# Kernel tuning notes

Measured on AMD Instinct MI355X. Metric: run time of the kernel, lower is better.

## Reference

```python
import jax, jax.numpy as jnp
import numpy as np

N, D, H, C, ED, E = 50000, 128, 8, 16, 16, 800000  # nodes, model dim, heads, head dim, edge dim, edges

def _layer_norm(x, g, b, eps=1e-5):
    mu = x.mean(-1, keepdims=True)
    var = ((x - mu) ** 2).mean(-1, keepdims=True)
    return (x - mu) * jax.lax.rsqrt(var + eps) * g + b

def setup_inputs() -> dict:
    key = jax.random.key(0)
    ks = jax.random.split(key, 24)
    s = 0.05
    inp = {
        'x': jax.random.normal(ks[0], (N, D), jnp.float32),
        'edge_index': jax.random.randint(ks[1], (2, E), 0, N, jnp.int32),
        'edge_attr': jax.random.normal(ks[2], (E, ED), jnp.float32),
        # TransformerConv params (Linear convention: y = x @ W + b)
        'wq': s * jax.random.normal(ks[3], (D, H * C)), 'bq': s * jax.random.normal(ks[4], (H * C,)),
        'wk': s * jax.random.normal(ks[5], (D, H * C)), 'bk': s * jax.random.normal(ks[6], (H * C,)),
        'wv': s * jax.random.normal(ks[7], (D, H * C)), 'bv': s * jax.random.normal(ks[8], (H * C,)),
        'we': s * jax.random.normal(ks[9], (ED, H * C)),            # lin_edge, bias=False
        'wskip': s * jax.random.normal(ks[10], (D, H * C)), 'bskip': s * jax.random.normal(ks[11], (H * C,)),
        'wbeta': s * jax.random.normal(ks[12], (3 * H * C, 1)),     # lin_beta, bias=False
        # norms
        'ln1_g': 1.0 + s * jax.random.normal(ks[13], (D,)), 'ln1_b': s * jax.random.normal(ks[14], (D,)),
        'ln2_g': 1.0 + s * jax.random.normal(ks[15], (D,)), 'ln2_b': s * jax.random.normal(ks[16], (D,)),
        # FFN
        'w1': s * jax.random.normal(ks[17], (D, 2 * D)), 'b1': s * jax.random.normal(ks[18], (2 * D,)),
        'w2': s * jax.random.normal(ks[19], (2 * D, D)), 'b2': s * jax.random.normal(ks[20], (D,)),
    }
    return inp

def reference(x, edge_index, edge_attr, wq, bq, wk, bk, wv, bv, we, wskip, bskip, wbeta,
              ln1_g, ln1_b, ln2_g, ln2_b, w1, b1, w2, b2):
    src, dst = edge_index[0], edge_index[1]  # message flows src (j) -> dst (i)
    # --- pre-norm + TransformerConv (beta=True, concat=True, eval-mode dropout=identity) ---
    xn = _layer_norm(x, ln1_g, ln1_b)
    q = (xn @ wq + bq).reshape(N, H, C)
    k = (xn @ wk + bk).reshape(N, H, C)
    v = (xn @ wv + bv).reshape(N, H, C)
    e = (edge_attr @ we).reshape(E, H, C)
    kj = k[src] + e                                     # [E,H,C]
    alpha = (q[dst] * kj).sum(-1) / jnp.sqrt(jnp.float32(C))  # [E,H]
    # segment softmax over incoming edges per destination node
    m = jax.ops.segment_max(alpha, dst, num_segments=N)        # [N,H]
    ea = jnp.exp(alpha - m[dst])
    denom = jax.ops.segment_sum(ea, dst, num_segments=N)
    alpha = ea / (denom[dst] + 1e-16)
    msg = (v[src] + e) * alpha[..., None]               # [E,H,C]
    out = jax.ops.segment_sum(msg, dst, num_segments=N).reshape(N, H * C)
    # beta-gated skip
    x_r = xn @ wskip + bskip
    beta = jax.nn.sigmoid(jnp.concatenate([out, x_r, out - x_r], axis=-1) @ wbeta)  # [N,1]
    out = beta * x_r + (1.0 - beta) * out
    x = x + out
    # --- pre-norm FFN ---
    h = _layer_norm(x, ln2_g, ln2_b)
    h = jax.nn.gelu(h @ w1 + b1, approximate=False) @ w2 + b2
    return x + h
```

## Files before the change

### kernel.cpp

```cpp
#include <hip/hip_runtime.h>
#include <math.h>

#define N_NODES 50000
#define D_MODEL 128
#define N_HEADS 8
#define HEAD_C 16
#define E_DIM 16
#define N_EDGES 800000

typedef __attribute__((ext_vector_type(8))) short bf16x8;
typedef __attribute__((ext_vector_type(4))) float f32x4;

__device__ inline ushort f2bf(float f) {
    unsigned u = __float_as_uint(f);
    unsigned r = (u + 0x7fffu + ((u >> 16) & 1u)) >> 16;
    return (ushort)r;
}
__device__ inline float bf2f(ushort h) { return __uint_as_float(((unsigned)h) << 16); }
__device__ inline uint pack2(float a, float b) {
    return (uint)f2bf(a) | ((uint)f2bf(b) << 16);
}
__device__ inline float gelu_f(float v) {
    return 0.5f * v * (1.0f + erff(v * 0.70710678118654752f));
}

__global__ void prep_weights(const float* __restrict__ wq, const float* __restrict__ wk,
                             const float* __restrict__ wv, const float* __restrict__ wsk,
                             const float* __restrict__ bq, const float* __restrict__ bk,
                             const float* __restrict__ bv, const float* __restrict__ bsk,
                             const float* __restrict__ w1, const float* __restrict__ w2,
                             ushort* __restrict__ wqkvsT, float* __restrict__ bqkvs,
                             ushort* __restrict__ w1T, ushort* __restrict__ w2T)
{
    int idx = blockIdx.x * 256 + threadIdx.x;
    {
        int m = idx >> 7, kk = idx & 127;
        int b = m >> 7, ch = m & 127;
        const float* src = (b == 0) ? wq : (b == 1) ? wk : (b == 2) ? wv : wsk;
        wqkvsT[idx] = f2bf(src[kk * 128 + ch]);
    }
    if (idx < 256 * 128) {
        int m = idx >> 7, k = idx & 127;
        w1T[idx] = f2bf(w1[k * 256 + m]);
    }
    if (idx < 128 * 256) {
        int m = idx >> 8, k = idx & 255;
        w2T[idx] = f2bf(w2[k * 128 + m]);
    }
    if (idx < 512) {
        int b = idx >> 7, ch = idx & 127;
        const float* bb = (b == 0) ? bq : (b == 1) ? bk : (b == 2) ? bv : bsk;
        bqkvs[idx] = bb[ch];
    }
}

__global__ __launch_bounds__(256) void proj_ln_gemm(
    const float* __restrict__ X, const float* __restrict__ ln_g, const float* __restrict__ ln_b,
    const ushort* __restrict__ WT, const float* __restrict__ bias,
    ushort* __restrict__ Y, int nrows)
{
    __shared__ __align__(16) ushort Al[128 * 128];
    __shared__ __align__(16) ushort Wl[64 * 128];
    int tid = threadIdx.x;
    int wv = tid >> 6, lane = tid & 63;
    int row0 = blockIdx.x * 128;
    int col0 = blockIdx.y * 64;

    int c16 = tid & 15;
    float4 g0 = *(const float4*)&ln_g[c16 * 8];
    float4 g1 = *(const float4*)&ln_g[c16 * 8 + 4];
    float4 bb0 = *(const float4*)&ln_b[c16 * 8];
    float4 bb1 = *(const float4*)&ln_b[c16 * 8 + 4];

    #pragma unroll
    for (int i = 0; i < 8; ++i) {
        int c = tid + i * 256;
        int r = c >> 4;
        int gr = row0 + r;
        float4 xa = make_float4(0.f, 0.f, 0.f, 0.f), xb = xa;
        if (gr < nrows) {
            xa = *(const float4*)&X[(size_t)gr * 128 + c16 * 8];
            xb = *(const float4*)&X[(size_t)gr * 128 + c16 * 8 + 4];
        }
        float s  = xa.x + xa.y + xa.z + xa.w + xb.x + xb.y + xb.z + xb.w;
        float ss = xa.x*xa.x + xa.y*xa.y + xa.z*xa.z + xa.w*xa.w
                 + xb.x*xb.x + xb.y*xb.y + xb.z*xb.z + xb.w*xb.w;
        #pragma unroll
        for (int m = 1; m < 16; m <<= 1) {
            s  += __shfl_xor(s,  m, 64);
            ss += __shfl_xor(ss, m, 64);
        }
        float mu  = s * (1.0f / 128.0f);
        float var = ss * (1.0f / 128.0f) - mu * mu;
        float rs  = rsqrtf(var + 1e-5f);
        ushort h[8];
        h[0] = f2bf((xa.x - mu) * rs * g0.x + bb0.x);
        h[1] = f2bf((xa.y - mu) * rs * g0.y + bb0.y);
        h[2] = f2bf((xa.z - mu) * rs * g0.z + bb0.z);
        h[3] = f2bf((xa.w - mu) * rs * g0.w + bb0.w);
        h[4] = f2bf((xb.x - mu) * rs * g1.x + bb1.x);
        h[5] = f2bf((xb.y - mu) * rs * g1.y + bb1.y);
        h[6] = f2bf((xb.z - mu) * rs * g1.z + bb1.z);
        h[7] = f2bf((xb.w - mu) * rs * g1.w + bb1.w);
        int byte = r * 256 + ((c16 * 16) ^ ((r & 7) << 4));
        *(ulonglong2*)((char*)Al + byte) = *(ulonglong2*)h;
    }
    #pragma unroll
    for (int i = 0; i < 4; ++i) {
        int c = tid + i * 256;
        int r = c >> 4, cc = c & 15;
        ulonglong2 val = *(const ulonglong2*)(WT + (size_t)(col0 + r) * 128 + cc * 8);
        int byte = r * 256 + ((cc * 16) ^ ((r & 7) << 4));
        *(ulonglong2*)((char*)Wl + byte) = val;
    }
    __syncthreads();

    f32x4 acc[2][4];
    #pragma unroll
    for (int i = 0; i < 2; ++i)
        #pragma unroll
        for (int j = 0; j < 4; ++j) acc[i][j] = (f32x4){0.f, 0.f, 0.f, 0.f};
    #pragma unroll
    for (int ks = 0; ks < 4; ++ks) {
        bf16x8 af[2], bfr[4];
        #pragma unroll
        for (int rt = 0; rt < 2; ++rt) {
            int r = wv * 32 + rt * 16 + (lane & 15);
            int byte = r * 256 + ((ks * 64 + (lane >> 4) * 16) ^ ((r & 7) << 4));
            af[rt] = *(const bf16x8*)((const char*)Al + byte);
        }
        #pragma unroll
        for (int ct = 0; ct < 4; ++ct) {
            int r = ct * 16 + (lane & 15);
            int byte = r * 256 + ((ks * 64 + (lane >> 4) * 16) ^ ((r & 7) << 4));
            bfr[ct] = *(const bf16x8*)((const char*)Wl + byte);
        }
        #pragma unroll
        for (int rt = 0; rt < 2; ++rt)
            #pragma unroll
            for (int ct = 0; ct < 4; ++ct)
                acc[rt][ct] = __builtin_amdgcn_mfma_f32_16x16x32_bf16(
                    af[rt], bfr[ct], acc[rt][ct], 0, 0, 0);
    }
    #pragma unroll
    for (int rt = 0; rt < 2; ++rt) {
        #pragma unroll
        for (int ct = 0; ct < 4; ++ct) {
            int gcol = col0 + ct * 16 + (lane & 15);
            float bv = bias[gcol];
            #pragma unroll
            for (int r = 0; r < 4; ++r) {
                int grow = row0 + wv * 32 + rt * 16 + (lane >> 4) * 4 + r;
                if (grow >= nrows) continue;
                Y[(size_t)grow * 512 + gcol] = f2bf(acc[rt][ct][r] + bv);
            }
        }
    }
}

__global__ __launch_bounds__(256) void ffn_fused(
    const ushort* __restrict__ A, const ushort* __restrict__ W1T,
    const ushort* __restrict__ W2T, const float* __restrict__ b1,
    const float* __restrict__ b2, const float* __restrict__ xnew,
    float* __restrict__ out, int nrows)
{
    __shared__ __align__(16) ushort Xl[128 * 128];
    __shared__ __align__(16) ushort Wl[64 * 256];
    __shared__ __align__(16) ushort Hl[128 * 256];
    int tid = threadIdx.x;
    int wv = tid >> 6, lane = tid & 63;
    int row0 = blockIdx.x * 128;

    #pragma unroll
    for (int i = 0; i < 8; ++i) {
        int c = tid + i * 256;
        int r = c >> 4, c16 = c & 15;
        int gr = row0 + r;
        ulonglong2 val = {0ull, 0ull};
        if (gr < nrows) val = *(const ulonglong2*)(A + (size_t)gr * 128 + c16 * 8);
        int byte = r * 256 + ((c16 * 16) ^ ((r & 7) << 4));
        *(ulonglong2*)((char*)Xl + byte) = val;
    }

    for (int h = 0; h < 2; ++h) {
        #pragma unroll
        for (int i = 0; i < 8; ++i) {
            int c = tid + i * 256;
            int r = c >> 4, c16 = c & 15;
            ulonglong2 val = *(const ulonglong2*)(W1T + (size_t)(h * 128 + r) * 128 + c16 * 8);
            int byte = r * 256 + ((c16 * 16) ^ ((r & 7) << 4));
            *(ulonglong2*)((char*)Wl + byte) = val;
        }
        __syncthreads();
        f32x4 acc1[2][8];
        #pragma unroll
        for (int i = 0; i < 2; ++i)
            #pragma unroll
            for (int j = 0; j < 8; ++j) acc1[i][j] = (f32x4){0.f, 0.f, 0.f, 0.f};
        #pragma unroll
        for (int ks = 0; ks < 4; ++ks) {
            bf16x8 af[2], bfr[8];
            #pragma unroll
            for (int rt = 0; rt < 2; ++rt) {
                int r = wv * 32 + rt * 16 + (lane & 15);
                int byte = r * 256 + ((ks * 64 + (lane >> 4) * 16) ^ ((r & 7) << 4));
                af[rt] = *(const bf16x8*)((const char*)Xl + byte);
            }
            #pragma unroll
            for (int ct = 0; ct < 8; ++ct) {
                int r = ct * 16 + (lane & 15);
                int byte = r * 256 + ((ks * 64 + (lane >> 4) * 16) ^ ((r & 7) << 4));
                bfr[ct] = *(const bf16x8*)((const char*)Wl + byte);
            }
            #pragma unroll
            for (int rt = 0; rt < 2; ++rt)
                #pragma unroll
                for (int ct = 0; ct < 8; ++ct)
                    acc1[rt][ct] = __builtin_amdgcn_mfma_f32_16x16x32_bf16(
                        af[rt], bfr[ct], acc1[rt][ct], 0, 0, 0);
        }
        #pragma unroll
        for (int rt = 0; rt < 2; ++rt) {
            #pragma unroll
            for (int ct = 0; ct < 8; ++ct) {
                int col = h * 128 + ct * 16 + (lane & 15);
                float bv = b1[col];
                #pragma unroll
                for (int r = 0; r < 4; ++r) {
                    int row = wv * 32 + rt * 16 + (lane >> 4) * 4 + r;
                    float v = gelu_f(acc1[rt][ct][r] + bv);
                    int cb = col * 2;
                    int byte = row * 512 + (((cb) & ~15) ^ ((row & 7) << 4)) + (cb & 15);
                    *(ushort*)((char*)Hl + byte) = f2bf(v);
                }
            }
        }
        __syncthreads();
    }

    for (int g = 0; g < 2; ++g) {
        #pragma unroll
        for (int i = 0; i < 8; ++i) {
            int c = tid + i * 256;
            int r = c >> 5, c32 = c & 31;
            ulonglong2 val = *(const ulonglong2*)(W2T + (size_t)(g * 64 + r) * 256 + c32 * 8);
            int byte = r * 512 + ((c32 * 16) ^ ((r & 7) << 4));
            *(ulonglong2*)((char*)Wl + byte) = val;
        }
        __syncthreads();
        f32x4 acc2[2][4];
        #pragma unroll
        for (int i = 0; i < 2; ++i)
            #pragma unroll
            for (int j = 0; j < 4; ++j) acc2[i][j] = (f32x4){0.f, 0.f, 0.f, 0.f};
        #pragma unroll
        for (int ks = 0; ks < 8; ++ks) {
            bf16x8 af[2], bfr[4];
            #pragma unroll
            for (int rt = 0; rt < 2; ++rt) {
                int row = wv * 32 + rt * 16 + (lane & 15);
                int byte = row * 512 + ((ks * 64 + (lane >> 4) * 16) ^ ((row & 7) << 4));
                af[rt] = *(const bf16x8*)((const char*)Hl + byte);
            }
            #pragma unroll
            for (int ct = 0; ct < 4; ++ct) {
                int r = ct * 16 + (lane & 15);
                int byte = r * 512 + ((ks * 64 + (lane >> 4) * 16) ^ ((r & 7) << 4));
                bfr[ct] = *(const bf16x8*)((const char*)Wl + byte);
            }
            #pragma unroll
            for (int rt = 0; rt < 2; ++rt)
                #pragma unroll
                for (int ct = 0; ct < 4; ++ct)
                    acc2[rt][ct] = __builtin_amdgcn_mfma_f32_16x16x32_bf16(
                        af[rt], bfr[ct], acc2[rt][ct], 0, 0, 0);
        }
        #pragma unroll
        for (int rt = 0; rt < 2; ++rt) {
            #pragma unroll
            for (int ct = 0; ct < 4; ++ct) {
                int gcol = g * 64 + ct * 16 + (lane & 15);
                float bv = b2[gcol];
                #pragma unroll
                for (int r = 0; r < 4; ++r) {
                    int grow = row0 + wv * 32 + rt * 16 + (lane >> 4) * 4 + r;
                    if (grow >= nrows) continue;
                    size_t idx = (size_t)grow * 128 + gcol;
                    out[idx] = acc2[rt][ct][r] + bv + xnew[idx];
                }
            }
        }
        __syncthreads();
    }
}

__global__ void hist_kernel(const int* __restrict__ dst, int* __restrict__ deg)
{
    int e = blockIdx.x * 256 + threadIdx.x;
    if (e < N_EDGES) atomicAdd(&deg[dst[e]], 1);
}

__global__ void scan1_kernel(const int* __restrict__ deg, int* __restrict__ off,
                             int* __restrict__ bsum)
{
    __shared__ int sm[256];
    int i = blockIdx.x * 256 + threadIdx.x;
    int v = (i < N_NODES) ? deg[i] : 0;
    sm[threadIdx.x] = v;
    __syncthreads();
    #pragma unroll
    for (int d = 1; d < 256; d <<= 1) {
        int t = (threadIdx.x >= d) ? sm[threadIdx.x - d] : 0;
        __syncthreads();
        sm[threadIdx.x] += t;
        __syncthreads();
    }
    if (i < N_NODES) off[i] = sm[threadIdx.x] - v;
    if (threadIdx.x == 255) bsum[blockIdx.x] = sm[255];
}

__global__ void scan2_kernel(int* __restrict__ bsum, int nb)
{
    __shared__ int sm[256];
    int v = (threadIdx.x < nb) ? bsum[threadIdx.x] : 0;
    sm[threadIdx.x] = v;
    __syncthreads();
    #pragma unroll
    for (int d = 1; d < 256; d <<= 1) {
        int t = (threadIdx.x >= d) ? sm[threadIdx.x - d] : 0;
        __syncthreads();
        sm[threadIdx.x] += t;
        __syncthreads();
    }
    if (threadIdx.x < nb) bsum[threadIdx.x] = sm[threadIdx.x] - v;
}

__global__ void scan3_kernel(int* __restrict__ off, const int* __restrict__ bsum,
                             int* __restrict__ cursor)
{
    int i = blockIdx.x * 256 + threadIdx.x;
    if (i < N_NODES) {
        int o = off[i] + bsum[blockIdx.x];
        off[i] = o;
        cursor[i] = o;
    }
}

__global__ void scatter_kernel(const int* __restrict__ dst, const int* __restrict__ src,
                               const float* __restrict__ eattr, int* __restrict__ cursor,
                               int* __restrict__ src_s, ushort* __restrict__ eattr_s)
{
    int e = blockIdx.x * 256 + threadIdx.x;
    if (e < N_EDGES) {
        int p = atomicAdd(&cursor[dst[e]], 1);
        src_s[p] = src[e];
        const float4* s4 = (const float4*)(eattr + (size_t)e * E_DIM);
        float4 f0 = s4[0], f1 = s4[1], f2 = s4[2], f3 = s4[3];
        uint4 u0, u1;
        u0.x = pack2(f0.x, f0.y); u0.y = pack2(f0.z, f0.w);
        u0.z = pack2(f1.x, f1.y); u0.w = pack2(f1.z, f1.w);
        u1.x = pack2(f2.x, f2.y); u1.y = pack2(f2.z, f2.w);
        u1.z = pack2(f3.x, f3.y); u1.w = pack2(f3.z, f3.w);
        uint4* d4 = (uint4*)(eattr_s + (size_t)p * E_DIM);
        d4[0] = u0; d4[1] = u1;
    }
}

#define ATTN_STEP(P, S, A0, A1, E0, E1) do {                                         \
    int sv_ = src_s[P];                                                              \
    uint eap_ = *(const uint*)(eattr_s + (size_t)(P) * E_DIM + j2);                  \
    float ea0_ = bf2f((ushort)eap_), ea1_ = bf2f((ushort)(eap_ >> 16));              \
    size_t sb_ = (size_t)sv_ * 512;                                                  \
    uint kp_ = *(const uint*)(qkvs + sb_ + 128 + 2 * lane);                          \
    uint vp_ = *(const uint*)(qkvs + sb_ + 256 + 2 * lane);                          \
    float p_ = q0 * bf2f((ushort)kp_) + q1 * bf2f((ushort)(kp_ >> 16))               \
             + ea0_ * qp0 + ea1_ * qp1;                                              \
    p_ += __shfl_xor(p_, 1, 64);                                                     \
    p_ += __shfl_xor(p_, 2, 64);                                                     \
    p_ += __shfl_xor(p_, 4, 64);                                                     \
    float w_ = __expf(fminf(p_, 60.f));                                              \
    S  += w_;                                                                        \
    A0 += w_ * bf2f((ushort)vp_);                                                    \
    A1 += w_ * bf2f((ushort)(vp_ >> 16));                                            \
    E0 += w_ * ea0_;                                                                 \
    E1 += w_ * ea1_;                                                                 \
} while (0)

__global__ void node_attn(const ushort* __restrict__ qkvs, const float* __restrict__ x,
                          const float* __restrict__ we, const float* __restrict__ wbeta,
                          const float* __restrict__ ln2g, const float* __restrict__ ln2b,
                          const int* __restrict__ off, const int* __restrict__ deg,
                          const int* __restrict__ src_s, const ushort* __restrict__ eattr_s,
                          float* __restrict__ xnew, ushort* __restrict__ h2)
{
    __shared__ float wl[E_DIM * 128];
    __shared__ float weT[128 * 17];
    __shared__ float sc4[4][128];
    for (int t = threadIdx.x; t < E_DIM * 32; t += 256)
        *(float4*)&wl[t * 4] = *(const float4*)&we[t * 4];
    for (int t = threadIdx.x; t < E_DIM * 128; t += 256) {
        int j = t >> 7, ch = t & 127;
        weT[ch * 17 + j] = we[t];
    }
    __syncthreads();

    int nl   = threadIdx.x >> 6;
    int node = blockIdx.x * 4 + nl;
    int lane = threadIdx.x & 63;
    if (node >= N_NODES) return;

    int j2 = (lane & 7) * 2;
    int hb = (lane >> 3) * 16;

    size_t nb = (size_t)node * 512;
    uint qp = *(const uint*)(qkvs + nb + 2 * lane);
    float q0r = bf2f((ushort)qp), q1r = bf2f((ushort)(qp >> 16));

    sc4[nl][2 * lane]     = q0r;
    sc4[nl][2 * lane + 1] = q1r;
    float qp0 = 0.f, qp1 = 0.f;
    #pragma unroll
    for (int c = 0; c < 16; ++c) {
        float qc = sc4[nl][hb + c];
        qp0 += qc * weT[(hb + c) * 17 + j2];
        qp1 += qc * weT[(hb + c) * 17 + j2 + 1];
    }
    float q0 = q0r * 0.25f, q1 = q1r * 0.25f;
    qp0 *= 0.25f; qp1 *= 0.25f;

    float SA = 0.f, A0a = 0.f, A1a = 0.f, E0a = 0.f, E1a = 0.f;
    float SB = 0.f, A0b = 0.f, A1b = 0.f, E0b = 0.f, E1b = 0.f;

    int o = off[node], dg = deg[node];
    int i = 0;
    for (; i + 2 <= dg; i += 2) {
        ATTN_STEP(o + i,     SA, A0a, A1a, E0a, E1a);
        ATTN_STEP(o + i + 1, SB, A0b, A1b, E0b, E1b);
    }
    if (i < dg)
        ATTN_STEP(o + i, SA, A0a, A1a, E0a, E1a);

    float S  = SA + SB;
    float A0 = A0a + A0b, A1 = A1a + A1b;
    float E0 = E0a + E0b, E1 = E1a + E1b;

    sc4[nl][2 * lane]     = E0;
    sc4[nl][2 * lane + 1] = E1;
    float ep0 = 0.f, ep1 = 0.f;
    #pragma unroll
    for (int j = 0; j < 16; ++j) {
        float es = sc4[nl][hb + j];
        ep0 += es * wl[j * 128 + 2 * lane];
        ep1 += es * wl[j * 128 + 2 * lane + 1];
    }

    float rinv = 1.f / (S + 1e-16f);
    float o0 = (A0 + ep0) * rinv;
    float o1 = (A1 + ep1) * rinv;

    uint xrp = *(const uint*)(qkvs + nb + 384 + 2 * lane);
    float xr0 = bf2f((ushort)xrp), xr1 = bf2f((ushort)(xrp >> 16));
    float2 wb0 = *(const float2*)&wbeta[2 * lane];
    float2 wb1 = *(const float2*)&wbeta[128 + 2 * lane];
    float2 wb2 = *(const float2*)&wbeta[256 + 2 * lane];
    float dot = o0 * wb0.x + o1 * wb0.y + xr0 * wb1.x + xr1 * wb1.y
              + (o0 - xr0) * wb2.x + (o1 - xr1) * wb2.y;
    #pragma unroll
    for (int w = 32; w > 0; w >>= 1) dot += __shfl_xor(dot, w, 64);
    float beta = 1.f / (1.f + __expf(-dot));

    size_t xb = (size_t)node * D_MODEL + 2 * lane;
    float2 xv = *(const float2*)&x[xb];
    float ox = xv.x + beta * xr0 + (1.f - beta) * o0;
    float oy = xv.y + beta * xr1 + (1.f - beta) * o1;
    *(float2*)&xnew[xb] = make_float2(ox, oy);

    float s2  = ox + oy;
    float ss2 = ox * ox + oy * oy;
    #pragma unroll
    for (int w = 32; w > 0; w >>= 1) {
        s2  += __shfl_xor(s2,  w, 64);
        ss2 += __shfl_xor(ss2, w, 64);
    }
    float mu  = s2 * (1.0f / 128.0f);
    float var = ss2 * (1.0f / 128.0f) - mu * mu;
    float rs  = rsqrtf(var + 1e-5f);
    float2 g2 = *(const float2*)&ln2g[2 * lane];
    float2 b2 = *(const float2*)&ln2b[2 * lane];
    float h0 = (ox - mu) * rs * g2.x + b2.x;
    float h1 = (oy - mu) * rs * g2.y + b2.y;
    ((uint*)h2)[(size_t)node * 64 + lane] = pack2(h0, h1);
}

extern "C" void kernel_launch(void* const* d_in, const int* in_sizes, int n_in,
                              void* d_out, int out_size, void* d_ws, size_t ws_size,
                              hipStream_t stream)
{
    const float* x     = (const float*)d_in[0];
    const int*   eidx  = (const int*)  d_in[1];
    const float* eattr = (const float*)d_in[2];
    const float* wq  = (const float*)d_in[3];  const float* bq  = (const float*)d_in[4];
    const float* wk  = (const float*)d_in[5];  const float* bk  = (const float*)d_in[6];
    const float* wv  = (const float*)d_in[7];  const float* bv  = (const float*)d_in[8];
    const float* we  = (const float*)d_in[9];
    const float* wsk = (const float*)d_in[10]; const float* bsk = (const float*)d_in[11];
    const float* wbeta = (const float*)d_in[12];
    const float* ln1g = (const float*)d_in[13]; const float* ln1b = (const float*)d_in[14];
    const float* ln2g = (const float*)d_in[15]; const float* ln2b = (const float*)d_in[16];
    const float* w1 = (const float*)d_in[17]; const float* b1 = (const float*)d_in[18];
    const float* w2 = (const float*)d_in[19]; const float* b2 = (const float*)d_in[20];
    const int* srcp = eidx;
    const int* dstp = eidx + N_EDGES;
    float* out = (float*)d_out;

    char* w = (char*)d_ws;
    size_t o = 0;
    ushort* qkvs_b  = (ushort*)(w + o);  o += (size_t)N_NODES * 512 * 2;
    float* xnew = (float*)(w + o);  o += (size_t)N_NODES * 128 * 4;
    ushort* eattr_s = (ushort*)(w + o); o += (size_t)N_EDGES * E_DIM * 2;
    int* src_s = (int*)(w + o);     o += (size_t)N_EDGES * 4;
    ushort* h2_b = (ushort*)(w + o); o += (size_t)N_NODES * 128 * 2;
    ushort* wqkvsT = (ushort*)(w + o); o += 512 * 128 * 2;
    ushort* w1T    = (ushort*)(w + o); o += 256 * 128 * 2;
    ushort* w2T    = (ushort*)(w + o); o += 128 * 256 * 2;
    float*  bqkvs  = (float*)(w + o);  o += 4096;
    int* deg    = (int*)(w + o); o += 200704;
    int* offb   = (int*)(w + o); o += 200704;
    int* cursor = (int*)(w + o); o += 200704;
    int* bsum   = (int*)(w + o); o += 4096;

    dim3 blk(256);
    dim3 lngrid((N_NODES + 3) / 4);
    const int NB = (N_NODES + 255) / 256;
    const int EB = (N_EDGES + 255) / 256;
    const int GB = (N_NODES + 127) / 128;

    prep_weights<<<dim3(256), blk, 0, stream>>>(wq, wk, wv, wsk, bq, bk, bv, bsk,
                                                w1, w2, wqkvsT, bqkvs, w1T, w2T);
    proj_ln_gemm<<<dim3(GB, 8), blk, 0, stream>>>(x, ln1g, ln1b, wqkvsT, bqkvs,
                                                  qkvs_b, N_NODES);
    hipMemsetAsync(deg, 0, (size_t)N_NODES * 4, stream);
    hist_kernel<<<dim3(EB), blk, 0, stream>>>(dstp, deg);
    scan1_kernel<<<dim3(NB), blk, 0, stream>>>(deg, offb, bsum);
    scan2_kernel<<<dim3(1), blk, 0, stream>>>(bsum, NB);
    scan3_kernel<<<dim3(NB), blk, 0, stream>>>(offb, bsum, cursor);
    scatter_kernel<<<dim3(EB), blk, 0, stream>>>(dstp, srcp, eattr, cursor, src_s, eattr_s);
    node_attn<<<lngrid, blk, 0, stream>>>(qkvs_b, x, we, wbeta, ln2g, ln2b,
                                          offb, deg, src_s, eattr_s, xnew, h2_b);
    ffn_fused<<<dim3(GB), blk, 0, stream>>>(h2_b, w1T, w2T, b1, b2, xnew, out, N_NODES);
}
```

Before: 320.5 us.

## Chunk FFN hidden dimension, widen projection tiles, fold degree memset into prep

New measurement: 293.9 us, median of 2. 1.09x faster.

```diff
diff --git a/kernel.cpp b/kernel.cpp
--- a/kernel.cpp
+++ b/kernel.cpp
@@ -30,7 +30,8 @@
                              const float* __restrict__ bv, const float* __restrict__ bsk,
                              const float* __restrict__ w1, const float* __restrict__ w2,
                              ushort* __restrict__ wqkvsT, float* __restrict__ bqkvs,
-                             ushort* __restrict__ w1T, ushort* __restrict__ w2T)
+                             ushort* __restrict__ w1T, ushort* __restrict__ w2T,
+                             int* __restrict__ deg)
 {
     int idx = blockIdx.x * 256 + threadIdx.x;
     {
@@ -52,6 +53,7 @@
         const float* bb = (b == 0) ? bq : (b == 1) ? bk : (b == 2) ? bv : bsk;
         bqkvs[idx] = bb[ch];
     }
+    if (idx < N_NODES) deg[idx] = 0;
 }
 
 __global__ __launch_bounds__(256) void proj_ln_gemm(
@@ -60,11 +62,11 @@
     ushort* __restrict__ Y, int nrows)
 {
     __shared__ __align__(16) ushort Al[128 * 128];
-    __shared__ __align__(16) ushort Wl[64 * 128];
+    __shared__ __align__(16) ushort Wl[128 * 128];
     int tid = threadIdx.x;
     int wv = tid >> 6, lane = tid & 63;
     int row0 = blockIdx.x * 128;
-    int col0 = blockIdx.y * 64;
+    int col0 = blockIdx.y * 128;
 
     int c16 = tid & 15;
     float4 g0 = *(const float4*)&ln_g[c16 * 8];
@@ -106,7 +108,7 @@
         *(ulonglong2*)((char*)Al + byte) = *(ulonglong2*)h;
     }
     #pragma unroll
-    for (int i = 0; i < 4; ++i) {
+    for (int i = 0; i < 8; ++i) {
         int c = tid + i * 256;
         int r = c >> 4, cc = c & 15;
         ulonglong2 val = *(const ulonglong2*)(WT + (size_t)(col0 + r) * 128 + cc * 8);
@@ -115,14 +117,14 @@
     }
     __syncthreads();
 
-    f32x4 acc[2][4];
+    f32x4 acc[2][8];
     #pragma unroll
     for (int i = 0; i < 2; ++i)
         #pragma unroll
-        for (int j = 0; j < 4; ++j) acc[i][j] = (f32x4){0.f, 0.f, 0.f, 0.f};
+        for (int j = 0; j < 8; ++j) acc[i][j] = (f32x4){0.f, 0.f, 0.f, 0.f};
     #pragma unroll
     for (int ks = 0; ks < 4; ++ks) {
-        bf16x8 af[2], bfr[4];
+        bf16x8 af[2], bfr[8];
         #pragma unroll
         for (int rt = 0; rt < 2; ++rt) {
             int r = wv * 32 + rt * 16 + (lane & 15);
@@ -130,7 +132,7 @@
             af[rt] = *(const bf16x8*)((const char*)Al + byte);
         }
         #pragma unroll
-        for (int ct = 0; ct < 4; ++ct) {
+        for (int ct = 0; ct < 8; ++ct) {
             int r = ct * 16 + (lane & 15);
             int byte = r * 256 + ((ks * 64 + (lane >> 4) * 16) ^ ((r & 7) << 4));
             bfr[ct] = *(const bf16x8*)((const char*)Wl + byte);
@@ -138,14 +140,14 @@
         #pragma unroll
         for (int rt = 0; rt < 2; ++rt)
             #pragma unroll
-            for (int ct = 0; ct < 4; ++ct)
+            for (int ct = 0; ct < 8; ++ct)
                 acc[rt][ct] = __builtin_amdgcn_mfma_f32_16x16x32_bf16(
                     af[rt], bfr[ct], acc[rt][ct], 0, 0, 0);
     }
     #pragma unroll
     for (int rt = 0; rt < 2; ++rt) {
         #pragma unroll
-        for (int ct = 0; ct < 4; ++ct) {
+        for (int ct = 0; ct < 8; ++ct) {
             int gcol = col0 + ct * 16 + (lane & 15);
             float bv = bias[gcol];
             #pragma unroll
@@ -165,8 +167,9 @@
     float* __restrict__ out, int nrows)
 {
     __shared__ __align__(16) ushort Xl[128 * 128];
-    __shared__ __align__(16) ushort Wl[64 * 256];
-    __shared__ __align__(16) ushort Hl[128 * 256];
+    __shared__ __align__(16) ushort W1l[64 * 128];
+    __shared__ __align__(16) ushort Hl[128 * 64];
+    __shared__ __align__(16) ushort W2l[128 * 64];
     int tid = threadIdx.x;
     int wv = tid >> 6, lane = tid & 63;
     int row0 = blockIdx.x * 128;
@@ -182,24 +185,39 @@
         *(ulonglong2*)((char*)Xl + byte) = val;
     }
 
-    for (int h = 0; h < 2; ++h) {
-        #pragma unroll
-        for (int i = 0; i < 8; ++i) {
+    f32x4 acc2[2][8];
+    #pragma unroll
+    for (int i = 0; i < 2; ++i)
+        #pragma unroll
+        for (int j = 0; j < 8; ++j) acc2[i][j] = (f32x4){0.f, 0.f, 0.f, 0.f};
+
+    for (int q = 0; q < 4; ++q) {
+        #pragma unroll
+        for (int i = 0; i < 4; ++i) {
             int c = tid + i * 256;
-            int r = c >> 4, c16 = c & 15;
-            ulonglong2 val = *(const ulonglong2*)(W1T + (size_t)(h * 128 + r) * 128 + c16 * 8);
-            int byte = r * 256 + ((c16 * 16) ^ ((r & 7) << 4));
-            *(ulonglong2*)((char*)Wl + byte) = val;
-        }
-        __syncthreads();
-        f32x4 acc1[2][8];
+            int r = c >> 4, cc = c & 15;
+            ulonglong2 val = *(const ulonglong2*)(W1T + (size_t)(q * 64 + r) * 128 + cc * 8);
+            int byte = r * 256 + ((cc * 16) ^ ((r & 7) << 4));
+            *(ulonglong2*)((char*)W1l + byte) = val;
+        }
+        #pragma unroll
+        for (int i = 0; i < 4; ++i) {
+            int c = tid + i * 256;
+            int r = c >> 3, c8 = c & 7;
+            ulonglong2 val = *(const ulonglong2*)(W2T + (size_t)r * 256 + q * 64 + c8 * 8);
+            int byte = r * 128 + ((c8 * 16) ^ ((r & 7) << 4));
+            *(ulonglong2*)((char*)W2l + byte) = val;
+        }
+        __syncthreads();
+
+        f32x4 acc1[2][4];
         #pragma unroll
         for (int i = 0; i < 2; ++i)
             #pragma unroll
-            for (int j = 0; j < 8; ++j) acc1[i][j] = (f32x4){0.f, 0.f, 0.f, 0.f};
+            for (int j = 0; j < 4; ++j) acc1[i][j] = (f32x4){0.f, 0.f, 0.f, 0.f};
         #pragma unroll
         for (int ks = 0; ks < 4; ++ks) {
-            bf16x8 af[2], bfr[8];
+            bf16x8 af[2], bfr[4];
             #pragma unroll
             for (int rt = 0; rt < 2; ++rt) {
                 int r = wv * 32 + rt * 16 + (lane & 15);
@@ -207,90 +225,75 @@
                 af[rt] = *(const bf16x8*)((const char*)Xl + byte);
             }
             #pragma unroll
-            for (int ct = 0; ct < 8; ++ct) {
+            for (int ct = 0; ct < 4; ++ct) {
                 int r = ct * 16 + (lane & 15);
                 int byte = r * 256 + ((ks * 64 + (lane >> 4) * 16) ^ ((r & 7) << 4));
-                bfr[ct] = *(const bf16x8*)((const char*)Wl + byte);
+                bfr[ct] = *(const bf16x8*)((const char*)W1l + byte);
             }
             #pragma unroll
             for (int rt = 0; rt < 2; ++rt)
                 #pragma unroll
-                for (int ct = 0; ct < 8; ++ct)
+                for (int ct = 0; ct < 4; ++ct)
                     acc1[rt][ct] = __builtin_amdgcn_mfma_f32_16x16x32_bf16(
                         af[rt], bfr[ct], acc1[rt][ct], 0, 0, 0);
         }
         #pragma unroll
         for (int rt = 0; rt < 2; ++rt) {
             #pragma unroll
-            for (int ct = 0; ct < 8; ++ct) {
-                int col = h * 128 + ct * 16 + (lane & 15);
-                float bv = b1[col];
+            for (int ct = 0; ct < 4; ++ct) {
+                int cl = ct * 16 + (lane & 15);
+                float bv = b1[q * 64 + cl];
                 #pragma unroll
                 for (int r = 0; r < 4; ++r) {
                     int row = wv * 32 + rt * 16 + (lane >> 4) * 4 + r;
                     float v = gelu_f(acc1[rt][ct][r] + bv);
-                    int cb = col * 2;
-                    int byte = row * 512 + (((cb) & ~15) ^ ((row & 7) << 4)) + (cb & 15);
+                    int cb = cl * 2;
+                    int byte = row * 128 + ((cb & ~15) ^ ((row & 7) << 4)) + (cb & 15);
                     *(ushort*)((char*)Hl + byte) = f2bf(v);
                 }
             }
         }
         __syncthreads();
-    }
-
-    for (int g = 0; g < 2; ++g) {
-        #pragma unroll
-        for (int i = 0; i < 8; ++i) {
-            int c = tid + i * 256;
-            int r = c >> 5, c32 = c & 31;
-            ulonglong2 val = *(const ulonglong2*)(W2T + (size_t)(g * 64 + r) * 256 + c32 * 8);
-            int byte = r * 512 + ((c32 * 16) ^ ((r & 7) << 4));
-            *(ulonglong2*)((char*)Wl + byte) = val;
-        }
-        __syncthreads();
-        f32x4 acc2[2][4];
-        #pragma unroll
-        for (int i = 0; i < 2; ++i)
-            #pragma unroll
-            for (int j = 0; j < 4; ++j) acc2[i][j] = (f32x4){0.f, 0.f, 0.f, 0.f};
-        #pragma unroll
-        for (int ks = 0; ks < 8; ++ks) {
-            bf16x8 af[2], bfr[4];
+
+        #pragma unroll
+        for (int ks = 0; ks < 2; ++ks) {
+            bf16x8 af[2], bfr[8];
             #pragma unroll
             for (int rt = 0; rt < 2; ++rt) {
                 int row = wv * 32 + rt * 16 + (lane & 15);
-                int byte = row * 512 + ((ks * 64 + (lane >> 4) * 16) ^ ((row & 7) << 4));
+                int byte = row * 128 + ((ks * 64 + (lane >> 4) * 16) ^ ((row & 7) << 4));
                 af[rt] = *(const bf16x8*)((const char*)Hl + byte);
             }
             #pragma unroll
-            for (int ct = 0; ct < 4; ++ct) {
+            for (int ct = 0; ct < 8; ++ct) {
                 int r = ct * 16 + (lane & 15);
-                int byte = r * 512 + ((ks * 64 + (lane >> 4) * 16) ^ ((r & 7) << 4));
-                bfr[ct] = *(const bf16x8*)((const char*)Wl + byte);
+                int byte = r * 128 + ((ks * 64 + (lane >> 4) * 16) ^ ((r & 7) << 4));
+                bfr[ct] = *(const bf16x8*)((const char*)W2l + byte);
             }
             #pragma unroll
             for (int rt = 0; rt < 2; ++rt)
                 #pragma unroll
-                for (int ct = 0; ct < 4; ++ct)
+                for (int ct = 0; ct < 8; ++ct)
                     acc2[rt][ct] = __builtin_amdgcn_mfma_f32_16x16x32_bf16(
                         af[rt], bfr[ct], acc2[rt][ct], 0, 0, 0);
         }
-        #pragma unroll
-        for (int rt = 0; rt < 2; ++rt) {
-            #pragma unroll
-            for (int ct = 0; ct < 4; ++ct) {
-                int gcol = g * 64 + ct * 16 + (lane & 15);
-                float bv = b2[gcol];
-                #pragma unroll
-                for (int r = 0; r < 4; ++r) {
-                    int grow = row0 + wv * 32 + rt * 16 + (lane >> 4) * 4 + r;
-                    if (grow >= nrows) continue;
-                    size_t idx = (size_t)grow * 128 + gcol;
-                    out[idx] = acc2[rt][ct][r] + bv + xnew[idx];
-                }
-            }
-        }
-        __syncthreads();
+        __syncthreads();
+    }
+
+    #pragma unroll
+    for (int rt = 0; rt < 2; ++rt) {
+        #pragma unroll
+        for (int ct = 0; ct < 8; ++ct) {
+            int gcol = ct * 16 + (lane & 15);
+            float bv = b2[gcol];
+            #pragma unroll
+            for (int r = 0; r < 4; ++r) {
+                int grow = row0 + wv * 32 + rt * 16 + (lane >> 4) * 4 + r;
+                if (grow >= nrows) continue;
+                size_t idx = (size_t)grow * 128 + gcol;
+                out[idx] = acc2[rt][ct][r] + bv + xnew[idx];
+            }
+        }
     }
 }
 
@@ -536,10 +539,9 @@
     const int GB = (N_NODES + 127) / 128;
 
     prep_weights<<<dim3(256), blk, 0, stream>>>(wq, wk, wv, wsk, bq, bk, bv, bsk,
-                                                w1, w2, wqkvsT, bqkvs, w1T, w2T);
-    proj_ln_gemm<<<dim3(GB, 8), blk, 0, stream>>>(x, ln1g, ln1b, wqkvsT, bqkvs,
+                                                w1, w2, wqkvsT, bqkvs, w1T, w2T, deg);
+    proj_ln_gemm<<<dim3(GB, 4), blk, 0, stream>>>(x, ln1g, ln1b, wqkvsT, bqkvs,
                                                   qkvs_b, N_NODES);
-    hipMemsetAsync(deg, 0, (size_t)N_NODES * 4, stream);
     hist_kernel<<<dim3(EB), blk, 0, stream>>>(dstp, deg);
     scan1_kernel<<<dim3(NB), blk, 0, stream>>>(deg, offb, bsum);
     scan2_kernel<<<dim3(1), blk, 0, stream>>>(bsum, NB);
```
